# Performance work log

Hardware: AMD Instinct MI355X
Metric: run time of the kernel (lower is better)

The kernel has to match this reference:

```python
import jax, jax.numpy as jnp
import numpy as np

SPECIES = (0, 1)
CUTOFF = 6.0
N_ATOMS, N_EDGES, N_TRIPLETS = 20000, 500000, 2000000

G2_ETAS = np.array([0.003214, 0.035711, 0.071421, 0.124987, 0.214264, 0.357106, 0.714213, 1.428426], dtype=np.float32)
G4_ETAS = np.array([0.000357, 0.028569, 0.089277], dtype=np.float32)
G4_ZETAS = np.array([1.0, 2.0, 4.0], dtype=np.float32)
G4_LMDAS = np.array([-1.0, 1.0], dtype=np.float32)


def setup_inputs() -> dict:
    key = jax.random.key(0)
    ks = jax.random.split(key, 6)
    atomic_numbers = jax.random.randint(ks[0], (N_ATOMS,), 0, 2, dtype=jnp.int32)
    edge_index = jax.random.randint(ks[1], (2, N_EDGES), 0, N_ATOMS, dtype=jnp.int32)
    D_st = jax.random.uniform(ks[2], (N_EDGES,), minval=0.5, maxval=6.5, dtype=jnp.float32)
    id3_ba = jax.random.randint(ks[3], (N_TRIPLETS,), 0, N_EDGES, dtype=jnp.int32)
    id3_ca = jax.random.randint(ks[4], (N_TRIPLETS,), 0, N_EDGES, dtype=jnp.int32)
    cosphi = jax.random.uniform(ks[5], (N_TRIPLETS,), minval=-1.0, maxval=1.0, dtype=jnp.float32)
    # per-key parameters: 4 ordered species pairs for G2, 6 species triples for G4
    g2_etas = jnp.tile(jnp.asarray(G2_ETAS), (4, 1))
    g4_etas = jnp.tile(jnp.asarray(G4_ETAS), (6, 1))
    g4_zetas = jnp.tile(jnp.asarray(G4_ZETAS), (6, 1))
    g4_lmdas = jnp.tile(jnp.asarray(G4_LMDAS), (6, 1))
    return {"atomic_numbers": atomic_numbers, "edge_index": edge_index, "D_st": D_st,
            "id3_ba": id3_ba, "id3_ca": id3_ca, "cosphi": cosphi,
            "g2_etas": g2_etas, "g4_etas": g4_etas, "g4_zetas": g4_zetas, "g4_lmdas": g4_lmdas}


def _fc(R):
    # cosine cutoff (no in-range bool here; G4 applies its own range masks)
    return 0.5 * jnp.cos(jnp.pi * R / CUTOFF) + 0.5


def _acsf(atomic_numbers, edge_index, D_st, id3_ba, id3_ca, cosphi,
          g2_etas, g4_etas, g4_zetas, g4_lmdas):
    N = atomic_numbers.shape[0]
    dt = D_st.dtype
    src, tgt = edge_index[0], edge_index[1]
    an_src, an_tgt = atomic_numbers[src], atomic_numbers[tgt]

    # ---- triplet geometry (masking replaces boolean gather; scatter-add is equivalent) ----
    m3 = id3_ba > id3_ca                       # [T] triplet dedup mask
    R_ba = D_st[id3_ba]                        # [T]
    R_ca = D_st[id3_ca]
    sb = atomic_numbers[src[id3_ba]]           # species of edge-ba source
    tb = atomic_numbers[tgt[id3_ba]]           # species of central atom a
    sc = atomic_numbers[src[id3_ca]]
    seg3 = tgt[id3_ba]                         # scatter target: central atom index
    Rbc2 = R_ba * R_ba + R_ca * R_ca - 2.0 * R_ba * R_ca * cosphi
    R_bc = jnp.sqrt(jnp.maximum(Rbc2, 1e-12))
    in_range = ((R_bc < CUTOFF) & (R_ba < CUTOFF) & (R_ca < CUTOFF)).astype(dt)
    cut3 = _fc(R_ca) * _fc(R_bc) * _fc(R_ba) * in_range   # [T]
    r2sum = R_bc * R_bc + R_ba * R_ba + R_ca * R_ca       # [T]

    # ---- G2: per (source, target) species pair ----
    cut2 = _fc(D_st)                           # [E]
    d2 = D_st * D_st
    g2_per = {}
    k = 0
    for a1 in SPECIES:
        for a2 in SPECIES:
            w = ((an_tgt == a2) & (an_src == a1)).astype(dt)       # [E]
            res = (cut2 * w)[:, None] * jnp.exp(-g2_etas[k][None, :] * d2[:, None])  # [E,8]
            g2_per[(a1, a2)] = jax.ops.segment_sum(res, tgt, num_segments=N)        # [N,8]
            k += 1

    # ---- G4: per (a, b, c) species triple (b<=c) ----
    ns = len(SPECIES)
    g4_per = {}
    k = 0
    for a in SPECIES:
        for i in range(ns):
            b = SPECIES[i]
            for j in range(i, ns):
                c = SPECIES[j]
                idx = (((sb == b) & (tb == a) & (sc == c)) |
                       ((sb == c) & (tb == a) & (sc == b)))
                w = (m3 & idx).astype(dt)                                  # [T]
                eta, zta, lmda = g4_etas[k], g4_zetas[k], g4_lmdas[k]
                rad = jnp.exp(-eta[None, :] * r2sum[:, None])              # [T,3]
                cl = jnp.abs(1.0 + lmda[None, :, None] * cosphi[:, None, None]) ** zta[None, None, :]  # [T,2,3]
                res = cl[:, None, :, :] * rad[:, :, None, None] * (cut3 * w)[:, None, None, None]      # [T,3,2,3]
                g4 = jax.ops.segment_sum(res, seg3, num_segments=N)        # [N,3,2,3]
                g4_per[(a, b, c)] = (2.0 ** (1.0 - zta))[None, None, None, :] * g4
                k += 1

    # ---- assemble per-atom descriptor [N, 70]; rows carry their species' descriptor ----
    outs = []
    for a in SPECIES:
        mask = (atomic_numbers == a).astype(dt)[:, None]
        g2s = jnp.stack([g2_per[(s, a)] for s in SPECIES], axis=-1).reshape(N, -1)   # [N,16]
        trips = [(b, c) for i, b in enumerate(SPECIES) for c in SPECIES[i:]]
        g4s = jnp.stack([g4_per[(a, b, c)] for (b, c) in trips], axis=-1).reshape(N, -1)  # [N,54]
        outs.append(mask * jnp.concatenate([g2s, g4s], axis=-1))
    return outs[0] + outs[1]


def reference(atomic_numbers, edge_index, D_st, id3_ba, id3_ca, cosphi,
              g2_etas, g4_etas, g4_zetas, g4_lmdas):
    return _acsf(atomic_numbers, edge_index, D_st, id3_ba, id3_ca, cosphi,
                 g2_etas, g4_etas, g4_zetas, g4_lmdas)
```

## Files before the change

### kernel.cpp

```cpp
#include <hip/hip_runtime.h>


#define CAP_T 96
#define CAP_E 64

typedef int    vi2 __attribute__((ext_vector_type(2)));
typedef int    vi4 __attribute__((ext_vector_type(4)));
typedef float  vf2 __attribute__((ext_vector_type(2)));
typedef float  vf4 __attribute__((ext_vector_type(4)));

static __device__ __forceinline__ float fc_dev(float R) {
    const float PI_OVER_CUT = 0.52359877559829887308f;
    return fmaf(0.5f, __cosf(PI_OVER_CUT * R), 0.5f);
}

static __device__ __forceinline__ unsigned enc_R(float d) {
    float u = rintf(d * (65535.0f / 8.0f));
    u = fminf(fmaxf(u, 0.0f), 65535.0f);
    return (unsigned)u;
}
static __device__ __forceinline__ float dec_R(unsigned pk) {
    return (float)(pk >> 16) * (8.0f / 65535.0f);
}


static __device__ __forceinline__ void process_edge(
        int e, float d, int src, int tgt,
        const int* __restrict__ an, const float* __restrict__ g2_etas,
        unsigned* __restrict__ epack, int* __restrict__ ecount,
        unsigned* __restrict__ erec, float* __restrict__ out) {
    int as = an[src];
    unsigned pk = (enc_R(d) << 16) | ((unsigned)tgt << 1) | (unsigned)as;
    epack[e] = pk;
    int slot = atomicAdd(&ecount[tgt], 1);
    if (slot < CAP_E) {
        erec[(size_t)tgt * CAP_E + slot] = pk;
    } else {
        float fcv = fc_dev(d), d2 = d * d;
        int at = an[tgt];
        const float* eta = g2_etas + (as * 2 + at) * 8;
        float* row = out + (size_t)tgt * 70 + as;
#pragma unroll
        for (int i = 0; i < 8; ++i)
            atomicAdd(row + 2 * i, fcv * __expf(-eta[i] * d2));
    }
}

__global__ void edges_bin_kernel(const int* __restrict__ an,
                                 const int* __restrict__ ei,
                                 const float* __restrict__ D,
                                 const float* __restrict__ g2_etas,
                                 unsigned* __restrict__ epack,
                                 int* __restrict__ ecount,
                                 unsigned* __restrict__ erec,
                                 float* __restrict__ out, int E) {
    int i = blockIdx.x * blockDim.x + threadIdx.x;
    int e0 = i * 2;
    if (e0 >= E) return;
    if (e0 + 1 < E) {
        vi2 sp = __builtin_nontemporal_load((const vi2*)ei + i);
        vi2 tp = __builtin_nontemporal_load((const vi2*)(ei + E) + i);
        vf2 dp = __builtin_nontemporal_load((const vf2*)D + i);
        process_edge(e0,     dp.x, sp.x, tp.x, an, g2_etas, epack, ecount, erec, out);
        process_edge(e0 + 1, dp.y, sp.y, tp.y, an, g2_etas, epack, ecount, erec, out);
    } else {
        process_edge(e0, D[e0], ei[e0], ei[E + e0], an, g2_etas, epack, ecount,
                     erec, out);
    }
}

static __device__ __forceinline__ void process_triplet(
        unsigned pb, unsigned pc, float cph,
        const int* __restrict__ an,
        const float* __restrict__ g4_etas,
        const float* __restrict__ g4_zetas,
        const float* __restrict__ g4_lmdas,
        int* __restrict__ tcount, vf2* __restrict__ trec,
        float* __restrict__ out) {
    float R_ba = dec_R(pb);
    float R_ca = dec_R(pc);
    if (R_ba >= 6.0f || R_ca >= 6.0f) return;
    float Rbc2 = R_ba * R_ba + R_ca * R_ca - 2.0f * R_ba * R_ca * cph;
    float Rm2 = fmaxf(Rbc2, 1e-12f);
    float R_bc = sqrtf(Rm2);
    if (R_bc >= 6.0f) return;
    int seg = (int)((pb >> 1) & 0x7FFFu);
    int trip = (int)(pb & 1u) + (int)(pc & 1u);
    float cut3 = fc_dev(R_ba) * fc_dev(R_ca) * fc_dev(R_bc);
    float r2sum = Rm2 + R_ba * R_ba + R_ca * R_ca;
    int slot = atomicAdd(&tcount[seg], 1);
    if (slot < CAP_T) {
        float cqf = fminf(fmaxf(fmaf(cph, 32767.5f, 32767.5f), 0.0f), 65535.0f);
        unsigned cq = (unsigned)rintf(cqf);
        unsigned c3q = (unsigned)rintf(cut3 * 16383.0f);
        unsigned w0 = (cq << 16) | (c3q << 2) | (unsigned)trip;
        vf2 r; r.x = __uint_as_float(w0); r.y = r2sum;
        trec[(size_t)seg * CAP_T + slot] = r;
    } else {
        int A = an[seg];
        int k4 = A * 3 + trip;
        const float* eta = g4_etas + k4 * 3;
        const float* zet = g4_zetas + k4 * 3;
        const float* lmd = g4_lmdas + k4 * 2;
        float rad[3];
#pragma unroll
        for (int e2 = 0; e2 < 3; ++e2)
            rad[e2] = __expf(-eta[e2] * r2sum) * cut3;
        float lg0 = __log2f(fabsf(fmaf(lmd[0], cph, 1.0f)));
        float lg1 = __log2f(fabsf(fmaf(lmd[1], cph, 1.0f)));
        float* row = out + (size_t)seg * 70 + 16 + trip;
#pragma unroll
        for (int z = 0; z < 3; ++z) {
            float zv = zet[z], base = 1.0f - zv;
            float c0 = exp2f(fmaf(zv, lg0, base));
            float c1 = exp2f(fmaf(zv, lg1, base));
#pragma unroll
            for (int e2 = 0; e2 < 3; ++e2) {
                atomicAdd(row + ((e2 * 2 + 0) * 3 + z) * 3, c0 * rad[e2]);
                atomicAdd(row + ((e2 * 2 + 1) * 3 + z) * 3, c1 * rad[e2]);
            }
        }
    }
}

__global__ void trip_bin_kernel(const unsigned* __restrict__ epack,
                                const int* __restrict__ id3_ba,
                                const int* __restrict__ id3_ca,
                                const float* __restrict__ cosphi,
                                const int* __restrict__ an,
                                const float* __restrict__ g4_etas,
                                const float* __restrict__ g4_zetas,
                                const float* __restrict__ g4_lmdas,
                                int* __restrict__ tcount,
                                vf2* __restrict__ trec,
                                float* __restrict__ out, int T) {
    int i = blockIdx.x * blockDim.x + threadIdx.x;
    int t0 = i * 4;
    if (t0 >= T) return;
    int ba[4], ca[4];
    float cp[4];
    if (t0 + 3 < T) {
        vi4 b4 = __builtin_nontemporal_load((const vi4*)id3_ba + i);
        vi4 c4 = __builtin_nontemporal_load((const vi4*)id3_ca + i);
        vf4 p4 = __builtin_nontemporal_load((const vf4*)cosphi + i);
        ba[0] = b4.x; ba[1] = b4.y; ba[2] = b4.z; ba[3] = b4.w;
        ca[0] = c4.x; ca[1] = c4.y; ca[2] = c4.z; ca[3] = c4.w;
        cp[0] = p4.x; cp[1] = p4.y; cp[2] = p4.z; cp[3] = p4.w;
    } else {
#pragma unroll
        for (int k = 0; k < 4; ++k) {
            int t = t0 + k;
            ba[k] = (t < T) ? id3_ba[t] : 0;
            ca[k] = (t < T) ? id3_ca[t] : 0;
            cp[k] = (t < T) ? cosphi[t] : 0.0f;
        }
    }
    unsigned pb[4], pc[4];
    bool m[4];
#pragma unroll
    for (int k = 0; k < 4; ++k) {
        m[k] = ba[k] > ca[k];
        pb[k] = 0u; pc[k] = 0u;
        if (m[k]) {
            pb[k] = epack[ba[k]];
            pc[k] = epack[ca[k]];
        }
    }
#pragma unroll
    for (int k = 0; k < 4; ++k) {
        if (m[k])
            process_triplet(pb[k], pc[k], cp[k], an, g4_etas, g4_zetas,
                            g4_lmdas, tcount, trec, out);
    }
}

__global__ __launch_bounds__(256) void gather_kernel(
        const int* __restrict__ an,
        const float* __restrict__ g2_etas,
        const float* __restrict__ g4_etas,
        const float* __restrict__ g4_zetas,
        const float* __restrict__ g4_lmdas,
        const int* __restrict__ tcount, const vf2* __restrict__ trec,
        const int* __restrict__ ecount, const unsigned* __restrict__ erec,
        float* __restrict__ out, int N) {
    __shared__ vf2      sg4[4][64];
    __shared__ unsigned sg2[4][64];
    int w = threadIdx.x >> 6;
    int lane = threadIdx.x & 63;
    int a = blockIdx.x * 4 + w;
    if (a >= N) return;
    int A = an[a];

    int trip_c = lane % 3;
    int z_c = (lane / 3) % 3;
    int l_c = (lane / 9) % 2;
    int e_c = lane / 18;
    float eta = 0.f, zv = 0.f, lm = 0.f, base = 1.f;
    if (lane < 54) {
        int k4 = A * 3 + trip_c;
        eta = g4_etas[k4 * 3 + e_c];
        zv  = g4_zetas[k4 * 3 + z_c];
        lm  = g4_lmdas[k4 * 2 + l_c];
        base = 1.0f - zv;
    }
    int n_t = min(tcount[a], CAP_T);
    const vf2* rec = trec + (size_t)a * CAP_T;
    float acc = 0.0f;
    for (int b0 = 0; b0 < n_t; b0 += 64) {
        int nch = min(64, n_t - b0);
        if (lane < nch) sg4[w][lane] = __builtin_nontemporal_load(rec + b0 + lane);
        for (int i = 0; i < nch; ++i) {
            vf2 b = sg4[w][i];
            unsigned w0 = __float_as_uint(b.x);
            int btr = (int)(w0 & 3u);
            float cut3 = (float)((w0 >> 2) & 0x3FFFu) * (1.0f / 16383.0f);
            float c = fmaf((float)(w0 >> 16), 2.0f / 65535.0f, -1.0f);
            float radv = __expf(-eta * b.y);
            float al = fabsf(fmaf(lm, c, 1.0f));
            float cl = exp2f(fmaf(zv, __log2f(al), base));
            acc += (btr == trip_c) ? cl * radv * cut3 : 0.0f;
        }
    }
    if (lane < 54) out[(size_t)a * 70 + 16 + lane] += acc;

    int s_c = lane & 1;
    int i_c = lane >> 1;
    float eta2 = (lane < 16) ? g2_etas[(s_c * 2 + A) * 8 + i_c] : 0.0f;
    int n_e = min(ecount[a], CAP_E);
    const unsigned* erc = erec + (size_t)a * CAP_E;
    float acc2 = 0.0f;
    for (int b0 = 0; b0 < n_e; b0 += 64) {
        int nch = min(64, n_e - b0);
        if (lane < nch) sg2[w][lane] = __builtin_nontemporal_load(erc + b0 + lane);
        for (int i = 0; i < nch; ++i) {
            unsigned pk = sg2[w][i];
            int sp = (int)(pk & 1u);
            float d = dec_R(pk);
            float v = fc_dev(d) * __expf(-eta2 * d * d);
            acc2 += (sp == s_c) ? v : 0.0f;
        }
    }
    if (lane < 16) out[(size_t)a * 70 + lane] += acc2;
}


__global__ void acsf_edges_kernel(const int* __restrict__ an,
                                  const int* __restrict__ ei,
                                  const float* __restrict__ D,
                                  const float* __restrict__ g2_etas,
                                  float2* __restrict__ edata,
                                  float* __restrict__ out,
                                  int E, int use_ws) {
    int e = blockIdx.x * blockDim.x + threadIdx.x;
    if (e >= E) return;
    float d = D[e];
    float cut2 = fc_dev(d);
    if (use_ws) edata[e] = make_float2(d, cut2);
    int src = ei[e];
    int tgt = ei[E + e];
    int as = an[src];
    int at = an[tgt];
    float d2 = d * d;
    const float* eta = g2_etas + (as * 2 + at) * 8;
    float* row = out + (size_t)tgt * 70 + as;
#pragma unroll
    for (int i = 0; i < 8; ++i)
        atomicAdd(row + 2 * i, cut2 * __expf(-eta[i] * d2));
}

__global__ void acsf_triplets_kernel(const int* __restrict__ an,
                                     const int* __restrict__ ei,
                                     const float* __restrict__ D,
                                     const float2* __restrict__ edata,
                                     const int* __restrict__ id3_ba,
                                     const int* __restrict__ id3_ca,
                                     const float* __restrict__ cosphi,
                                     const float* __restrict__ g4_etas,
                                     const float* __restrict__ g4_zetas,
                                     const float* __restrict__ g4_lmdas,
                                     float* __restrict__ out,
                                     int T, int E, int use_ws) {
    int t = blockIdx.x * blockDim.x + threadIdx.x;
    if (t >= T) return;
    int eba = id3_ba[t];
    int eca = id3_ca[t];
    if (eba <= eca) return;
    float R_ba, R_ca, fba, fca;
    if (use_ws) {
        float2 va = edata[eba];
        float2 vb = edata[eca];
        R_ba = va.x; fba = va.y;
        R_ca = vb.x; fca = vb.y;
    } else {
        R_ba = D[eba]; R_ca = D[eca];
        fba = fc_dev(R_ba); fca = fc_dev(R_ca);
    }
    if (R_ba >= 6.0f || R_ca >= 6.0f) return;
    float cph = cosphi[t];
    float Rbc2 = R_ba * R_ba + R_ca * R_ca - 2.0f * R_ba * R_ca * cph;
    float Rm2 = fmaxf(Rbc2, 1e-12f);
    float R_bc = sqrtf(Rm2);
    if (R_bc >= 6.0f) return;
    int seg = ei[E + eba];
    int A = an[seg];
    int sb = an[ei[eba]];
    int sc = an[ei[eca]];
    int trip = sb + sc;
    int k4 = A * 3 + trip;
    float cut3 = fba * fca * fc_dev(R_bc);
    float r2sum = Rm2 + R_ba * R_ba + R_ca * R_ca;
    const float* eta = g4_etas + k4 * 3;
    const float* zet = g4_zetas + k4 * 3;
    const float* lmd = g4_lmdas + k4 * 2;
    float rad[3];
#pragma unroll
    for (int e2 = 0; e2 < 3; ++e2)
        rad[e2] = __expf(-eta[e2] * r2sum) * cut3;
    float lg0 = __log2f(fabsf(fmaf(lmd[0], cph, 1.0f)));
    float lg1 = __log2f(fabsf(fmaf(lmd[1], cph, 1.0f)));
    float* row = out + (size_t)seg * 70 + 16 + trip;
#pragma unroll
    for (int z = 0; z < 3; ++z) {
        float zv = zet[z], bse = 1.0f - zv;
        float c0 = exp2f(fmaf(zv, lg0, bse));
        float c1 = exp2f(fmaf(zv, lg1, bse));
#pragma unroll
        for (int e2 = 0; e2 < 3; ++e2) {
            atomicAdd(row + ((e2 * 2 + 0) * 3 + z) * 3, c0 * rad[e2]);
            atomicAdd(row + ((e2 * 2 + 1) * 3 + z) * 3, c1 * rad[e2]);
        }
    }
}


extern "C" void kernel_launch(void* const* d_in, const int* in_sizes, int n_in,
                              void* d_out, int out_size, void* d_ws, size_t ws_size,
                              hipStream_t stream) {
    const int*   an       = (const int*)d_in[0];
    const int*   ei       = (const int*)d_in[1];
    const float* D        = (const float*)d_in[2];
    const int*   id3_ba   = (const int*)d_in[3];
    const int*   id3_ca   = (const int*)d_in[4];
    const float* cosphi   = (const float*)d_in[5];
    const float* g2_etas  = (const float*)d_in[6];
    const float* g4_etas  = (const float*)d_in[7];
    const float* g4_zetas = (const float*)d_in[8];
    const float* g4_lmdas = (const float*)d_in[9];
    (void)n_in;

    int N = in_sizes[0];
    int E = in_sizes[2];
    int T = in_sizes[3];
    float* out = (float*)d_out;

    size_t trec_b  = (size_t)N * CAP_T * sizeof(vf2);
    size_t epack_b = (size_t)((E + 1) & ~1) * sizeof(unsigned);
    size_t erec_b  = (size_t)N * CAP_E * sizeof(unsigned);
    size_t cnt_b   = (size_t)N * sizeof(int) * 2;
    size_t need = trec_b + epack_b + erec_b + cnt_b;

    const int blk = 256;
    (void)hipMemsetAsync(d_out, 0, (size_t)out_size * sizeof(float), stream);

    if (ws_size >= need && N <= 32767) {
        char* p = (char*)d_ws;
        vf2*      trec  = (vf2*)p;             p += trec_b;
        unsigned* epack = (unsigned*)p;        p += epack_b;
        unsigned* erec  = (unsigned*)p;        p += erec_b;
        int*      tcount = (int*)p;
        int*      ecount = tcount + N;
        (void)hipMemsetAsync(tcount, 0, cnt_b, stream);

        int ethreads = (E + 1) / 2;
        edges_bin_kernel<<<(ethreads + blk - 1) / blk, blk, 0, stream>>>(
            an, ei, D, g2_etas, epack, ecount, erec, out, E);
        int tthreads = (T + 3) / 4;
        trip_bin_kernel<<<(tthreads + blk - 1) / blk, blk, 0, stream>>>(
            epack, id3_ba, id3_ca, cosphi, an,
            g4_etas, g4_zetas, g4_lmdas, tcount, trec, out, T);
        gather_kernel<<<(N + 3) / 4, blk, 0, stream>>>(
            an, g2_etas, g4_etas, g4_zetas, g4_lmdas,
            tcount, trec, ecount, erec, out, N);
    } else {
        int use_ws = (ws_size >= (size_t)E * sizeof(float2)) ? 1 : 0;
        float2* edata = (float2*)d_ws;
        acsf_edges_kernel<<<(E + blk - 1) / blk, blk, 0, stream>>>(
            an, ei, D, g2_etas, edata, out, E, use_ws);
        acsf_triplets_kernel<<<(T + blk - 1) / blk, blk, 0, stream>>>(
            an, ei, D, edata, id3_ba, id3_ca, cosphi,
            g4_etas, g4_zetas, g4_lmdas, out, T, E, use_ws);
    }
}
```

Before: 209.3 us.

## Spread gather loop work across idle lanes and specialize integer zeta powers

The gather kernel now has each wavefront lane hold parameters for all three triplet species and process a third of the triplet records, then combines the partial sums with shuffles. This uses lanes that were idle and cuts the number of serial iterations. When zeta is 1, 2 or 4 it replaces exp2/log2 with multiplications. The G2 pass splits edges across four lane groups and reads a cutoff value quantized to 15 bits and precomputed in the edge binning kernel, which adds quantization error to the result.

```diff
diff --git a/kernel.cpp b/kernel.cpp
--- a/kernel.cpp
+++ b/kernel.cpp
@@ -30,13 +30,15 @@
         unsigned* __restrict__ epack, int* __restrict__ ecount,
         unsigned* __restrict__ erec, float* __restrict__ out) {
     int as = an[src];
-    unsigned pk = (enc_R(d) << 16) | ((unsigned)tgt << 1) | (unsigned)as;
-    epack[e] = pk;
+    unsigned dq = enc_R(d);
+    epack[e] = (dq << 16) | ((unsigned)tgt << 1) | (unsigned)as;
+    float fcv = fc_dev(d);
     int slot = atomicAdd(&ecount[tgt], 1);
     if (slot < CAP_E) {
-        erec[(size_t)tgt * CAP_E + slot] = pk;
-    } else {
-        float fcv = fc_dev(d), d2 = d * d;
+        unsigned fq = (unsigned)rintf(fminf(fmaxf(fcv, 0.0f), 1.0f) * 32767.0f);
+        erec[(size_t)tgt * CAP_E + slot] = (dq << 16) | (fq << 1) | (unsigned)as;
+    } else {
+        float d2 = d * d;
         int at = an[tgt];
         const float* eta = g2_etas + (as * 2 + at) * 8;
         float* row = out + (size_t)tgt * 70 + as;
@@ -183,7 +185,7 @@
         const int* __restrict__ tcount, const vf2* __restrict__ trec,
         const int* __restrict__ ecount, const unsigned* __restrict__ erec,
         float* __restrict__ out, int N) {
-    __shared__ vf2      sg4[4][64];
+    __shared__ vf2      sg4[4][66];
     __shared__ unsigned sg2[4][64];
     int w = threadIdx.x >> 6;
     int lane = threadIdx.x & 63;
@@ -191,56 +193,118 @@
     if (a >= N) return;
     int A = an[a];
 
-    int trip_c = lane % 3;
-    int z_c = (lane / 3) % 3;
-    int l_c = (lane / 9) % 2;
-    int e_c = lane / 18;
-    float eta = 0.f, zv = 0.f, lm = 0.f, base = 1.f;
-    if (lane < 54) {
-        int k4 = A * 3 + trip_c;
-        eta = g4_etas[k4 * 3 + e_c];
-        zv  = g4_zetas[k4 * 3 + z_c];
-        lm  = g4_lmdas[k4 * 2 + l_c];
-        base = 1.0f - zv;
-    }
+    int c18 = lane % 18;
+    int g3  = lane / 18;
+    int g3r = (g3 > 2) ? 0 : g3;
+    int z_c = c18 % 3;
+    int l_c = (c18 / 3) % 2;
+    int e_c = c18 / 6;
+    float eta0, eta1, eta2w, zv0, zv1, zv2, lm0, lm1, lm2;
+    {
+        int k0 = A * 3 + 0, k1 = A * 3 + 1, k2 = A * 3 + 2;
+        eta0 = g4_etas[k0 * 3 + e_c]; eta1 = g4_etas[k1 * 3 + e_c]; eta2w = g4_etas[k2 * 3 + e_c];
+        zv0  = g4_zetas[k0 * 3 + z_c]; zv1 = g4_zetas[k1 * 3 + z_c]; zv2 = g4_zetas[k2 * 3 + z_c];
+        lm0  = g4_lmdas[k0 * 2 + l_c]; lm1 = g4_lmdas[k1 * 2 + l_c]; lm2 = g4_lmdas[k2 * 2 + l_c];
+    }
+    auto zsel = [](float z) -> int {
+        return (z == 1.0f) ? 0 : (z == 2.0f) ? 1 : (z == 4.0f) ? 2 : 3;
+    };
+    int zs0 = zsel(zv0), zs1 = zsel(zv1), zs2 = zsel(zv2);
+    bool fastz = __all(zs0 < 3 && zs1 < 3 && zs2 < 3);
+
     int n_t = min(tcount[a], CAP_T);
     const vf2* rec = trec + (size_t)a * CAP_T;
-    float acc = 0.0f;
+    float acc0 = 0.0f, acc1 = 0.0f, acc2 = 0.0f;
+    vf2 zr; zr.x = 0.0f; zr.y = 0.0f;
     for (int b0 = 0; b0 < n_t; b0 += 64) {
         int nch = min(64, n_t - b0);
-        if (lane < nch) sg4[w][lane] = __builtin_nontemporal_load(rec + b0 + lane);
-        for (int i = 0; i < nch; ++i) {
-            vf2 b = sg4[w][i];
-            unsigned w0 = __float_as_uint(b.x);
-            int btr = (int)(w0 & 3u);
-            float cut3 = (float)((w0 >> 2) & 0x3FFFu) * (1.0f / 16383.0f);
-            float c = fmaf((float)(w0 >> 16), 2.0f / 65535.0f, -1.0f);
-            float radv = __expf(-eta * b.y);
-            float al = fabsf(fmaf(lm, c, 1.0f));
-            float cl = exp2f(fmaf(zv, __log2f(al), base));
-            acc += (btr == trip_c) ? cl * radv * cut3 : 0.0f;
-        }
-    }
-    if (lane < 54) out[(size_t)a * 70 + 16 + lane] += acc;
-
-    int s_c = lane & 1;
-    int i_c = lane >> 1;
-    float eta2 = (lane < 16) ? g2_etas[(s_c * 2 + A) * 8 + i_c] : 0.0f;
+        vf2 rv = zr;
+        if (lane < nch) rv = __builtin_nontemporal_load(rec + b0 + lane);
+        sg4[w][lane] = rv;
+        if (lane < 2) sg4[w][64 + lane] = zr;
+        asm volatile("s_waitcnt lgkmcnt(0)" ::: "memory");
+        int niter = (nch + 2) / 3;
+        if (fastz) {
+            for (int i = 0; i < niter; ++i) {
+                vf2 b = sg4[w][i * 3 + g3r];
+                unsigned w0 = __float_as_uint(b.x);
+                int btr = (int)(w0 & 3u);
+                float cut3 = (float)((w0 >> 2) & 0x3FFFu) * (1.0f / 16383.0f);
+                float c = fmaf((float)(w0 >> 16), 2.0f / 65535.0f, -1.0f);
+                float eta_r = (btr == 0) ? eta0 : (btr == 1) ? eta1 : eta2w;
+                float lm_r  = (btr == 0) ? lm0  : (btr == 1) ? lm1  : lm2;
+                int   zs_r  = (btr == 0) ? zs0  : (btr == 1) ? zs1  : zs2;
+                float p1 = fabsf(fmaf(lm_r, c, 1.0f));
+                float p2 = p1 * p1;
+                float p4 = p2 * p2;
+                float cl = (zs_r == 0) ? p1 : (zs_r == 1) ? p2 * 0.5f : p4 * 0.125f;
+                float v = cl * __expf(-eta_r * b.y) * cut3;
+                acc0 += (btr == 0) ? v : 0.0f;
+                acc1 += (btr == 1) ? v : 0.0f;
+                acc2 += (btr == 2) ? v : 0.0f;
+            }
+        } else {
+            for (int i = 0; i < niter; ++i) {
+                vf2 b = sg4[w][i * 3 + g3r];
+                unsigned w0 = __float_as_uint(b.x);
+                int btr = (int)(w0 & 3u);
+                float cut3 = (float)((w0 >> 2) & 0x3FFFu) * (1.0f / 16383.0f);
+                float c = fmaf((float)(w0 >> 16), 2.0f / 65535.0f, -1.0f);
+                float eta_r = (btr == 0) ? eta0 : (btr == 1) ? eta1 : eta2w;
+                float lm_r  = (btr == 0) ? lm0  : (btr == 1) ? lm1  : lm2;
+                float zv_r  = (btr == 0) ? zv0  : (btr == 1) ? zv1  : zv2;
+                float p1 = fabsf(fmaf(lm_r, c, 1.0f));
+                float cl = exp2f(fmaf(zv_r, __log2f(p1), 1.0f - zv_r));
+                float v = cl * __expf(-eta_r * b.y) * cut3;
+                acc0 += (btr == 0) ? v : 0.0f;
+                acc1 += (btr == 1) ? v : 0.0f;
+                acc2 += (btr == 2) ? v : 0.0f;
+            }
+        }
+    }
+    {
+        int cc = lane / 3;
+        int tt = lane - cc * 3;
+        float s0a = __shfl(acc0, cc),      s1a = __shfl(acc1, cc),      s2a = __shfl(acc2, cc);
+        float s0b = __shfl(acc0, cc + 18), s1b = __shfl(acc1, cc + 18), s2b = __shfl(acc2, cc + 18);
+        float s0c = __shfl(acc0, cc + 36), s1c = __shfl(acc1, cc + 36), s2c = __shfl(acc2, cc + 36);
+        float va = (tt == 0) ? s0a : (tt == 1) ? s1a : s2a;
+        float vb = (tt == 0) ? s0b : (tt == 1) ? s1b : s2b;
+        float vc = (tt == 0) ? s0c : (tt == 1) ? s1c : s2c;
+        if (lane < 54) out[(size_t)a * 70 + 16 + lane] += va + vb + vc;
+    }
+
+    int c16 = lane & 15;
+    int g4g = lane >> 4;
+    int s_c = c16 & 1;
+    int i_c = c16 >> 1;
+    float eta2 = g2_etas[(s_c * 2 + A) * 8 + i_c];
     int n_e = min(ecount[a], CAP_E);
     const unsigned* erc = erec + (size_t)a * CAP_E;
-    float acc2 = 0.0f;
+    float accg = 0.0f;
     for (int b0 = 0; b0 < n_e; b0 += 64) {
         int nch = min(64, n_e - b0);
-        if (lane < nch) sg2[w][lane] = __builtin_nontemporal_load(erc + b0 + lane);
-        for (int i = 0; i < nch; ++i) {
-            unsigned pk = sg2[w][i];
+        unsigned rv = 0u;
+        if (lane < nch) rv = __builtin_nontemporal_load(erc + b0 + lane);
+        sg2[w][lane] = rv;
+        asm volatile("s_waitcnt lgkmcnt(0)" ::: "memory");
+        int niter = (nch + 3) / 4;
+        for (int i = 0; i < niter; ++i) {
+            unsigned pk = sg2[w][i * 4 + g4g];
             int sp = (int)(pk & 1u);
             float d = dec_R(pk);
-            float v = fc_dev(d) * __expf(-eta2 * d * d);
-            acc2 += (sp == s_c) ? v : 0.0f;
-        }
-    }
-    if (lane < 16) out[(size_t)a * 70 + lane] += acc2;
+            float fcv = (float)((pk >> 1) & 0x7FFFu) * (1.0f / 32767.0f);
+            float v = fcv * __expf(-eta2 * d * d);
+            accg += (sp == s_c) ? v : 0.0f;
+        }
+    }
+    {
+        float r0 = __shfl(accg, lane);
+        float r1 = __shfl(accg, lane + 16);
+        float r2 = __shfl(accg, lane + 32);
+        float r3 = __shfl(accg, lane + 48);
+        if (lane < 16) out[(size_t)a * 70 + lane] += r0 + r1 + r2 + r3;
+    }
 }
 
 
```

Measured after the change: 186.6 us. 10.8% less time.
